# Optimization experiments

Hardware: AMD Instinct MI355X
Metric: run time of the kernel (lower is better)

## Reference

```python
import jax, jax.numpy as jnp
import numpy as np

CONF_THR = 0.2      # confidence_threshold default
NMS_THR = 0.45      # nms_threshold default
TARGET_ID = 0       # NAME2ID['person'] in COCO ordering
CLASS_OFFSET = 1e4  # per-class box offset so cross-class IoU == 0 (per-class NMS)
B, N, C = 4, 8192, 80


def setup_inputs() -> dict:
    key = jax.random.key(0)
    kxy, kwh, kobj, kcls = jax.random.split(key, 4)
    xy = jax.random.uniform(kxy, (B, N, 2)) * 600.0          # x1, y1
    wh = jax.random.uniform(kwh, (B, N, 2)) * 100.0 + 1.0    # box w, h
    boxes = jnp.concatenate([xy, xy + wh], axis=-1)           # x1 y1 x2 y2
    obj = jax.random.uniform(kobj, (B, N, 1))                 # objectness score
    clsp = jax.random.uniform(kcls, (B, N, C))                # class probs
    detection = jnp.concatenate([boxes, obj, clsp], axis=-1)  # [B, N, 5+C]
    return {"detection": detection}


def _pairwise_iou(b):
    # b: [N, 4] in x1y1x2y2
    area = (b[:, 2] - b[:, 0]) * (b[:, 3] - b[:, 1])
    lt = jnp.maximum(b[:, None, :2], b[None, :, :2])
    rb = jnp.minimum(b[:, None, 2:], b[None, :, 2:])
    wh = jnp.clip(rb - lt, 0.0)
    inter = wh[..., 0] * wh[..., 1]
    return inter / (area[:, None] + area[None, :] - inter + 1e-9)


def _nms_image(boxes, scores, classprobs, labels):
    # Fixed-shape, masked equivalent of the torch per-image filter+per-class NMS.
    valid = (scores > CONF_THR) & (labels == TARGET_ID)
    s = jnp.where(valid, scores, -1.0)
    order = jnp.argsort(-s)  # descending score (NMS visiting order)
    b = boxes[order]
    s = s[order]
    cp = classprobs[order]
    lb = labels[order]
    v = valid[order]
    # Offset boxes per class label -> IoU between different classes is 0,
    # which exactly reproduces the per-class NMS loop.
    ob = b + lb.astype(b.dtype)[:, None] * CLASS_OFFSET
    iou = _pairwise_iou(ob)  # [N, N]

    def step(keep, xs):
        row, i, vi = xs
        suppressed = jnp.any(keep & (row > NMS_THR))
        k = vi & jnp.logical_not(suppressed)
        return keep.at[i].set(k), k

    _, keep = jax.lax.scan(
        step, jnp.zeros(s.shape[0], dtype=bool), (iou, jnp.arange(s.shape[0]), v)
    )
    # Compact kept detections to the front (stable sort preserves descending score
    # order among kept boxes, matching the final argsort in torch).
    s_rank = jnp.where(keep, s, -1.0)
    final = jnp.argsort(-s_rank)
    kf = keep[final]
    m = kf.astype(b.dtype)
    out_boxes = b[final] * m[:, None]
    out_scores = jnp.where(kf, s[final], 0.0)
    out_classprobs = cp[final] * m
    out_labels = jnp.where(kf, lb[final], -1)
    return out_boxes, out_scores, out_classprobs, out_labels


def reference(detection):
    # split_detections
    boxes = detection[..., :4]           # [B, N, 4]
    scores = detection[..., 4]           # [B, N]
    cls = detection[..., 5:]             # [B, N, C]
    classprobs = jnp.max(cls, axis=-1)
    labels = jnp.argmax(cls, axis=-1)
    # filter_detections, batched over images
    return jax.vmap(_nms_image)(boxes, scores, classprobs, labels)
```

## Files before the change

### kernel.cpp

```cpp
#include <hip/hip_runtime.h>
#include <cstdint>
#include <cstddef>

typedef unsigned long long u64;

#define BB 4
#define NN 8192
#define DSTRIDE 85
#define RPB 64
#define BPI 128
#define NBLK (BB * BPI)
#define RCAP 64
#define SCAP 256
#define CONF_THRF 0.2f
#define NMS_THRF 0.45f
#define PLANE (BB * NN)

__global__ __launch_bounds__(256) void scan_kernel(
    const float* __restrict__ det, float* __restrict__ out,
    int* __restrict__ counts, float* __restrict__ cand) {
  __shared__ int wcnt[4];
  const int tid = threadIdx.x;
  const int blk = blockIdx.x;
  const int r = tid >> 2, q = tid & 3;
  const int row = blk * RPB + r;
  const float* d = det + (size_t)row * DSTRIDE;

  float best = -1.0f; int barg = 0;
  const float* cb = d + 5 + 20 * q;
#pragma unroll
  for (int k = 0; k < 5; ++k) {
    float4 v = *reinterpret_cast<const float4*>(cb + 4 * k);
    int c0 = 20 * q + 4 * k;
    if (v.x > best) { best = v.x; barg = c0; }
    if (v.y > best) { best = v.y; barg = c0 + 1; }
    if (v.z > best) { best = v.z; barg = c0 + 2; }
    if (v.w > best) { best = v.w; barg = c0 + 3; }
  }
#pragma unroll
  for (int off = 1; off <= 2; off <<= 1) {
    float ov = __shfl_xor(best, off);
    int   oa = __shfl_xor(barg, off);
    if (ov > best || (ov == best && oa < barg)) { best = ov; barg = oa; }
  }

  float4 box = make_float4(0.f, 0.f, 0.f, 0.f);
  float score = 0.f;
  bool valid = false;
  if (q == 0) {
    box = *reinterpret_cast<const float4*>(d);
    score = d[4];
    valid = (score > CONF_THRF) && (barg == 0);
  }

  const int base = blk * RPB;
  if (tid < 64) {
    reinterpret_cast<float4*>(out)[base + tid] = make_float4(0.f, 0.f, 0.f, 0.f);
  } else if (tid < 128) {
    out[(size_t)PLANE * 4 + base + (tid - 64)] = 0.f;
  } else if (tid < 192) {
    out[(size_t)PLANE * 5 + base + (tid - 128)] = 0.f;
  } else {
    out[(size_t)PLANE * 6 + base + (tid - 192)] = -1.0f;
  }

  u64 mask = __ballot(valid);
  const int wave = tid >> 6, lane = tid & 63;
  if (lane == 0) wcnt[wave] = __popcll(mask);
  __syncthreads();
  if (valid) {
    int offw = (wave > 0 ? wcnt[0] : 0) + (wave > 1 ? wcnt[1] : 0) +
               (wave > 2 ? wcnt[2] : 0);
    int pos = __popcll(mask & ((1ull << lane) - 1ull));
    float* p = cand + ((size_t)blk * RCAP + (offw + pos)) * 8;
    reinterpret_cast<float4*>(p)[0] = box;
    reinterpret_cast<float4*>(p)[1] =
        make_float4(score, best, __int_as_float(row & (NN - 1)), 0.f);
  }
  if (tid == 0) counts[blk] = wcnt[0] + wcnt[1] + wcnt[2] + wcnt[3];
}

__global__ __launch_bounds__(256) void nms_kernel(
    float* __restrict__ out, const int* __restrict__ counts,
    const float* __restrict__ cand) {
  __shared__ int cnt[BPI];
  __shared__ float ux1[SCAP], uy1[SCAP], ux2[SCAP], uy2[SCAP];
  __shared__ float usc[SCAP], ucp[SCAP];
  __shared__ u64 keys[SCAP];
  __shared__ float sx1[SCAP], sy1[SCAP], sx2[SCAP], sy2[SCAP];
  __shared__ float sar[SCAP], ssc[SCAP], scp[SCAP];
  __shared__ u64 mat[SCAP][4];

  const int b = blockIdx.x, tid = threadIdx.x;

  int c0 = 0;
  if (tid < BPI) { c0 = counts[b * BPI + tid]; cnt[tid] = c0; }
  __syncthreads();
  for (int s = 1; s < BPI; s <<= 1) {
    int v = 0;
    if (tid < BPI) { v = cnt[tid]; if (tid >= s) v += cnt[tid - s]; }
    __syncthreads();
    if (tid < BPI) cnt[tid] = v;
    __syncthreads();
  }
  int K = cnt[BPI - 1];
  if (K > SCAP) K = SCAP;

  if (tid < BPI && c0 > 0) {
    int off = cnt[tid] - c0;
    const float4* p = reinterpret_cast<const float4*>(
        cand + ((size_t)(b * BPI + tid)) * RCAP * 8);
    for (int k = 0; k < c0; ++k) {
      int o = off + k;
      if (o < SCAP) {
        float4 v0 = p[2 * k], v1 = p[2 * k + 1];
        ux1[o] = v0.x; uy1[o] = v0.y; ux2[o] = v0.z; uy2[o] = v0.w;
        usc[o] = v1.x; ucp[o] = v1.y;
        int idx = __float_as_int(v1.z);
        keys[o] = ((u64)__float_as_uint(v1.x) << 32) |
                  ((u64)(unsigned)(0xFFFF - idx) << 16) | (unsigned)o;
      }
    }
  }
  __syncthreads();

  if (tid < K) {
    u64 my = keys[tid];
    int r = 0;
    for (int s = 0; s < K; ++s) r += (keys[s] > my) ? 1 : 0;
    float x1 = ux1[tid], y1 = uy1[tid], x2 = ux2[tid], y2 = uy2[tid];
    sx1[r] = x1; sy1[r] = y1; sx2[r] = x2; sy2[r] = y2;
    sar[r] = (x2 - x1) * (y2 - y1);
    ssc[r] = usc[tid]; scp[r] = ucp[tid];
  }
  __syncthreads();

  const int W = (K + 63) >> 6;
  for (int t = tid; t < K * 4; t += 256) {
    int i = t >> 2, w = t & 3;
    u64 word = 0;
    if (w < W) {
      float ax1 = sx1[i], ay1 = sy1[i], ax2 = sx2[i], ay2 = sy2[i], aa = sar[i];
      int j0 = w * 64;
      int jend = min(K, j0 + 64);
      for (int j = max(j0, i + 1); j < jend; ++j) {
        float xx1 = fmaxf(ax1, sx1[j]);
        float yy1 = fmaxf(ay1, sy1[j]);
        float xx2 = fminf(ax2, sx2[j]);
        float yy2 = fminf(ay2, sy2[j]);
        float wi = fmaxf(xx2 - xx1, 0.f);
        float hi = fmaxf(yy2 - yy1, 0.f);
        float inter = wi * hi;
        float iou = inter / (aa + sar[j] - inter + 1e-9f);
        if (iou > NMS_THRF) word |= 1ull << (j - j0);
      }
    }
    mat[i][w] = word;
  }
  __syncthreads();

  u64 rem0 = 0, rem1 = 0, rem2 = 0, rem3 = 0;
  u64 kp0 = 0, kp1 = 0, kp2 = 0, kp3 = 0;
#define GREEDY_CHUNK(WW, REMW, KPW)                                        \
  for (int ii = 0; ii < 64; ++ii) {                                        \
    int i = (WW) * 64 + ii;                                                \
    if (i >= K) break;                                                     \
    u64 m0 = mat[i][0], m1 = mat[i][1], m2 = mat[i][2], m3 = mat[i][3];    \
    if (!((REMW >> ii) & 1ull)) {                                          \
      KPW |= 1ull << ii;                                                   \
      rem0 |= m0; rem1 |= m1; rem2 |= m2; rem3 |= m3;                      \
    }                                                                      \
  }
  GREEDY_CHUNK(0, rem0, kp0)
  GREEDY_CHUNK(1, rem1, kp1)
  GREEDY_CHUNK(2, rem2, kp2)
  GREEDY_CHUNK(3, rem3, kp3)
#undef GREEDY_CHUNK

  if (tid < K) {
    int wi = tid >> 6, bi = tid & 63;
    u64 kw = (wi == 0) ? kp0 : (wi == 1) ? kp1 : (wi == 2) ? kp2 : kp3;
    if ((kw >> bi) & 1ull) {
      int r = (wi > 0 ? __popcll(kp0) : 0) + (wi > 1 ? __popcll(kp1) : 0) +
              (wi > 2 ? __popcll(kp2) : 0) +
              __popcll(kw & ((1ull << bi) - 1ull));
      size_t o = (size_t)b * NN + r;
      reinterpret_cast<float4*>(out)[o] =
          make_float4(sx1[tid], sy1[tid], sx2[tid], sy2[tid]);
      out[(size_t)PLANE * 4 + o] = ssc[tid];
      out[(size_t)PLANE * 5 + o] = scp[tid];
      out[(size_t)PLANE * 6 + o] = 0.0f;
    }
  }
}

extern "C" void kernel_launch(void* const* d_in, const int* in_sizes, int n_in,
                              void* d_out, int out_size, void* d_ws, size_t ws_size,
                              hipStream_t stream) {
  const float* det = (const float*)d_in[0];
  float* out = (float*)d_out;
  int* counts = (int*)d_ws;
  float* cand = (float*)((char*)d_ws + 2048);

  scan_kernel<<<NBLK, 256, 0, stream>>>(det, out, counts, cand);
  nms_kernel<<<BB, 256, 0, stream>>>(out, counts, cand);
}
```

Before: 84.41 us.

## Fuse scan and NMS into one kernel with last-block flag wait

Merges the per-row scan and the per-image NMS into a single launch. Each block publishes its candidate count with a marker through an atomic release store, and the last block then polls these flags and runs NMS for all four images, one wave per image, synchronising with wave barriers only. Input rows are staged through LDS before the class argmax, and the candidate cap drops from 256 to 192. The aim is to remove the second launch and the inter-kernel gap. The cost is that all NMS work is serialised onto one block, and the fixed marker is never cleared between calls, so stale flags in the workspace can let the last block read counts before this call's blocks have written them.

```diff
diff --git a/kernel.cpp b/kernel.cpp
--- a/kernel.cpp
+++ b/kernel.cpp
@@ -11,48 +11,62 @@
 #define BPI 128
 #define NBLK (BB * BPI)
 #define RCAP 64
-#define SCAP 256
+#define SCAP 192
 #define CONF_THRF 0.2f
 #define NMS_THRF 0.45f
 #define PLANE (BB * NN)
-
-__global__ __launch_bounds__(256) void scan_kernel(
+#define IMSZ 16640
+#define MARK 0x5EED
+
+__device__ __forceinline__ void wave_fence() {
+  __asm__ volatile("" ::: "memory");
+  __builtin_amdgcn_wave_barrier();
+  __asm__ volatile("" ::: "memory");
+}
+
+__global__ __launch_bounds__(256) void fused_kernel(
     const float* __restrict__ det, float* __restrict__ out,
     int* __restrict__ counts, float* __restrict__ cand) {
+  __shared__ __align__(16) char arena[4 * IMSZ];
   __shared__ int wcnt[4];
   const int tid = threadIdx.x;
   const int blk = blockIdx.x;
+  const int wave = tid >> 6, lane = tid & 63;
+
+  {
+    const float4* src =
+        reinterpret_cast<const float4*>(det + (size_t)blk * (RPB * DSTRIDE));
+    float4* dst = reinterpret_cast<float4*>(arena);
+    for (int i = tid; i < (RPB * DSTRIDE) / 4; i += 256) dst[i] = src[i];
+  }
+  __syncthreads();
+
+  const float* st = reinterpret_cast<const float*>(arena);
   const int r = tid >> 2, q = tid & 3;
-  const int row = blk * RPB + r;
-  const float* d = det + (size_t)row * DSTRIDE;
-
   float best = -1.0f; int barg = 0;
-  const float* cb = d + 5 + 20 * q;
-#pragma unroll
-  for (int k = 0; k < 5; ++k) {
-    float4 v = *reinterpret_cast<const float4*>(cb + 4 * k);
-    int c0 = 20 * q + 4 * k;
-    if (v.x > best) { best = v.x; barg = c0; }
-    if (v.y > best) { best = v.y; barg = c0 + 1; }
-    if (v.z > best) { best = v.z; barg = c0 + 2; }
-    if (v.w > best) { best = v.w; barg = c0 + 3; }
+  {
+    const float* rowp = st + r * DSTRIDE + 5 + 20 * q;
+#pragma unroll
+    for (int k = 0; k < 20; ++k) {
+      float v = rowp[k];
+      if (v > best) { best = v; barg = 20 * q + k; }
+    }
   }
 #pragma unroll
   for (int off = 1; off <= 2; off <<= 1) {
     float ov = __shfl_xor(best, off);
-    int   oa = __shfl_xor(barg, off);
+    int oa = __shfl_xor(barg, off);
     if (ov > best || (ov == best && oa < barg)) { best = ov; barg = oa; }
   }
-
   float4 box = make_float4(0.f, 0.f, 0.f, 0.f);
   float score = 0.f;
   bool valid = false;
   if (q == 0) {
-    box = *reinterpret_cast<const float4*>(d);
-    score = d[4];
+    const float* rp = st + r * DSTRIDE;
+    box = make_float4(rp[0], rp[1], rp[2], rp[3]);
+    score = rp[4];
     valid = (score > CONF_THRF) && (barg == 0);
   }
-
   const int base = blk * RPB;
   if (tid < 64) {
     reinterpret_cast<float4*>(out)[base + tid] = make_float4(0.f, 0.f, 0.f, 0.f);
@@ -63,132 +77,157 @@
   } else {
     out[(size_t)PLANE * 6 + base + (tid - 192)] = -1.0f;
   }
-
   u64 mask = __ballot(valid);
-  const int wave = tid >> 6, lane = tid & 63;
   if (lane == 0) wcnt[wave] = __popcll(mask);
   __syncthreads();
+  int bcount = wcnt[0] + wcnt[1] + wcnt[2] + wcnt[3];
   if (valid) {
     int offw = (wave > 0 ? wcnt[0] : 0) + (wave > 1 ? wcnt[1] : 0) +
                (wave > 2 ? wcnt[2] : 0);
     int pos = __popcll(mask & ((1ull << lane) - 1ull));
-    float* p = cand + ((size_t)blk * RCAP + (offw + pos)) * 8;
-    reinterpret_cast<float4*>(p)[0] = box;
-    reinterpret_cast<float4*>(p)[1] =
-        make_float4(score, best, __int_as_float(row & (NN - 1)), 0.f);
-  }
-  if (tid == 0) counts[blk] = wcnt[0] + wcnt[1] + wcnt[2] + wcnt[3];
-}
-
-__global__ __launch_bounds__(256) void nms_kernel(
-    float* __restrict__ out, const int* __restrict__ counts,
-    const float* __restrict__ cand) {
-  __shared__ int cnt[BPI];
-  __shared__ float ux1[SCAP], uy1[SCAP], ux2[SCAP], uy2[SCAP];
-  __shared__ float usc[SCAP], ucp[SCAP];
-  __shared__ u64 keys[SCAP];
-  __shared__ float sx1[SCAP], sy1[SCAP], sx2[SCAP], sy2[SCAP];
-  __shared__ float sar[SCAP], ssc[SCAP], scp[SCAP];
-  __shared__ u64 mat[SCAP][4];
-
-  const int b = blockIdx.x, tid = threadIdx.x;
-
-  int c0 = 0;
-  if (tid < BPI) { c0 = counts[b * BPI + tid]; cnt[tid] = c0; }
+    float4* p =
+        reinterpret_cast<float4*>(cand + ((size_t)blk * RCAP + offw + pos) * 8);
+    p[0] = box;
+    p[1] = make_float4(score, best,
+                       __int_as_float((blk & (BPI - 1)) * RPB + r), 0.f);
+  }
   __syncthreads();
-  for (int s = 1; s < BPI; s <<= 1) {
-    int v = 0;
-    if (tid < BPI) { v = cnt[tid]; if (tid >= s) v += cnt[tid - s]; }
-    __syncthreads();
-    if (tid < BPI) cnt[tid] = v;
-    __syncthreads();
-  }
-  int K = cnt[BPI - 1];
+  if (tid == 0)
+    __hip_atomic_store(&counts[blk], (MARK << 16) | bcount, __ATOMIC_RELEASE,
+                       __HIP_MEMORY_SCOPE_AGENT);
+
+  if (blk != NBLK - 1) return;
+
+  const int img = wave;
+  char* A = arena + img * IMSZ;
+  u64* keys = reinterpret_cast<u64*>(A);
+  u64* mat = reinterpret_cast<u64*>(A + 1536);
+  float* ux1 = reinterpret_cast<float*>(A + 6144);
+  float* uy1 = reinterpret_cast<float*>(A + 6912);
+  float* ux2 = reinterpret_cast<float*>(A + 7680);
+  float* uy2 = reinterpret_cast<float*>(A + 8448);
+  float* usc = reinterpret_cast<float*>(A + 9216);
+  float* ucp = reinterpret_cast<float*>(A + 9984);
+  float* sx1 = reinterpret_cast<float*>(A + 10752);
+  float* sy1 = reinterpret_cast<float*>(A + 11520);
+  float* sx2 = reinterpret_cast<float*>(A + 12288);
+  float* sy2 = reinterpret_cast<float*>(A + 13056);
+  float* sar = reinterpret_cast<float*>(A + 13824);
+  float* ssc = reinterpret_cast<float*>(A + 14592);
+  float* scp = reinterpret_cast<float*>(A + 15360);
+
+  const int m0 = img * BPI + lane, m1 = m0 + 64;
+  int v0, v1;
+  do {
+    v0 = __hip_atomic_load(&counts[m0], __ATOMIC_ACQUIRE,
+                           __HIP_MEMORY_SCOPE_AGENT);
+  } while ((v0 >> 16) != MARK);
+  do {
+    v1 = __hip_atomic_load(&counts[m1], __ATOMIC_ACQUIRE,
+                           __HIP_MEMORY_SCOPE_AGENT);
+  } while ((v1 >> 16) != MARK);
+  int c0 = v0 & 0xFFFF, c1 = v1 & 0xFFFF;
+
+  int s0 = c0;
+#pragma unroll
+  for (int d = 1; d < 64; d <<= 1) {
+    int t = __shfl_up(s0, d);
+    if (lane >= d) s0 += t;
+  }
+  int tot0 = __shfl(s0, 63);
+  int s1 = c1;
+#pragma unroll
+  for (int d = 1; d < 64; d <<= 1) {
+    int t = __shfl_up(s1, d);
+    if (lane >= d) s1 += t;
+  }
+  s1 += tot0;
+  int K = __shfl(s1, 63);
   if (K > SCAP) K = SCAP;
-
-  if (tid < BPI && c0 > 0) {
-    int off = cnt[tid] - c0;
-    const float4* p = reinterpret_cast<const float4*>(
-        cand + ((size_t)(b * BPI + tid)) * RCAP * 8);
-    for (int k = 0; k < c0; ++k) {
-      int o = off + k;
+  int e0 = s0 - c0, e1 = s1 - c1;
+
+#pragma unroll
+  for (int pass = 0; pass < 2; ++pass) {
+    int m = pass ? m1 : m0;
+    int c = pass ? c1 : c0;
+    int e = pass ? e1 : e0;
+    const float4* p = reinterpret_cast<const float4*>(cand + (size_t)m * RCAP * 8);
+    for (int k = 0; k < c; ++k) {
+      int o = e + k;
       if (o < SCAP) {
-        float4 v0 = p[2 * k], v1 = p[2 * k + 1];
-        ux1[o] = v0.x; uy1[o] = v0.y; ux2[o] = v0.z; uy2[o] = v0.w;
-        usc[o] = v1.x; ucp[o] = v1.y;
-        int idx = __float_as_int(v1.z);
-        keys[o] = ((u64)__float_as_uint(v1.x) << 32) |
+        float4 a = p[2 * k], bq = p[2 * k + 1];
+        ux1[o] = a.x; uy1[o] = a.y; ux2[o] = a.z; uy2[o] = a.w;
+        usc[o] = bq.x; ucp[o] = bq.y;
+        int idx = __float_as_int(bq.z);
+        keys[o] = ((u64)__float_as_uint(bq.x) << 32) |
                   ((u64)(unsigned)(0xFFFF - idx) << 16) | (unsigned)o;
       }
     }
   }
-  __syncthreads();
-
-  if (tid < K) {
-    u64 my = keys[tid];
-    int r = 0;
-    for (int s = 0; s < K; ++s) r += (keys[s] > my) ? 1 : 0;
-    float x1 = ux1[tid], y1 = uy1[tid], x2 = ux2[tid], y2 = uy2[tid];
-    sx1[r] = x1; sy1[r] = y1; sx2[r] = x2; sy2[r] = y2;
-    sar[r] = (x2 - x1) * (y2 - y1);
-    ssc[r] = usc[tid]; scp[r] = ucp[tid];
-  }
-  __syncthreads();
-
-  const int W = (K + 63) >> 6;
-  for (int t = tid; t < K * 4; t += 256) {
-    int i = t >> 2, w = t & 3;
-    u64 word = 0;
-    if (w < W) {
-      float ax1 = sx1[i], ay1 = sy1[i], ax2 = sx2[i], ay2 = sy2[i], aa = sar[i];
-      int j0 = w * 64;
-      int jend = min(K, j0 + 64);
-      for (int j = max(j0, i + 1); j < jend; ++j) {
-        float xx1 = fmaxf(ax1, sx1[j]);
-        float yy1 = fmaxf(ay1, sy1[j]);
-        float xx2 = fminf(ax2, sx2[j]);
-        float yy2 = fminf(ay2, sy2[j]);
-        float wi = fmaxf(xx2 - xx1, 0.f);
-        float hi = fmaxf(yy2 - yy1, 0.f);
-        float inter = wi * hi;
-        float iou = inter / (aa + sar[j] - inter + 1e-9f);
-        if (iou > NMS_THRF) word |= 1ull << (j - j0);
+  wave_fence();
+
+  for (int o = lane; o < K; o += 64) {
+    u64 my = keys[o];
+    int rr = 0;
+    for (int s = 0; s < K; ++s) rr += (keys[s] > my) ? 1 : 0;
+    float x1 = ux1[o], y1 = uy1[o], x2 = ux2[o], y2 = uy2[o];
+    sx1[rr] = x1; sy1[rr] = y1; sx2[rr] = x2; sy2[rr] = y2;
+    sar[rr] = (x2 - x1) * (y2 - y1);
+    ssc[rr] = usc[o]; scp[rr] = ucp[o];
+  }
+  wave_fence();
+
+  for (int i = lane; i < K; i += 64) {
+    float ax1 = sx1[i], ay1 = sy1[i], ax2 = sx2[i], ay2 = sy2[i], aa = sar[i];
+    u64 w0 = 0, w1 = 0, w2 = 0;
+    for (int j = i + 1; j < K; ++j) {
+      float xx1 = fmaxf(ax1, sx1[j]);
+      float yy1 = fmaxf(ay1, sy1[j]);
+      float xx2 = fminf(ax2, sx2[j]);
+      float yy2 = fminf(ay2, sy2[j]);
+      float w = fmaxf(xx2 - xx1, 0.f);
+      float h = fmaxf(yy2 - yy1, 0.f);
+      float inter = w * h;
+      float iou = inter / (aa + sar[j] - inter + 1e-9f);
+      if (iou > NMS_THRF) {
+        u64 bit = 1ull << (j & 63);
+        int wj = j >> 6;
+        w0 |= (wj == 0) ? bit : 0;
+        w1 |= (wj == 1) ? bit : 0;
+        w2 |= (wj == 2) ? bit : 0;
       }
     }
-    mat[i][w] = word;
-  }
-  __syncthreads();
-
-  u64 rem0 = 0, rem1 = 0, rem2 = 0, rem3 = 0;
-  u64 kp0 = 0, kp1 = 0, kp2 = 0, kp3 = 0;
-#define GREEDY_CHUNK(WW, REMW, KPW)                                        \
-  for (int ii = 0; ii < 64; ++ii) {                                        \
-    int i = (WW) * 64 + ii;                                                \
-    if (i >= K) break;                                                     \
-    u64 m0 = mat[i][0], m1 = mat[i][1], m2 = mat[i][2], m3 = mat[i][3];    \
-    if (!((REMW >> ii) & 1ull)) {                                          \
-      KPW |= 1ull << ii;                                                   \
-      rem0 |= m0; rem1 |= m1; rem2 |= m2; rem3 |= m3;                      \
-    }                                                                      \
+    mat[i * 3] = w0; mat[i * 3 + 1] = w1; mat[i * 3 + 2] = w2;
+  }
+  wave_fence();
+
+  u64 rem0 = 0, rem1 = 0, rem2 = 0, kp0 = 0, kp1 = 0, kp2 = 0;
+#define GREEDY_CHUNK(WW, REMW, KPW)                                      \
+  for (int ii = 0; ii < 64; ++ii) {                                      \
+    int i = (WW) * 64 + ii;                                              \
+    if (i >= K) break;                                                   \
+    u64 g0 = mat[i * 3], g1 = mat[i * 3 + 1], g2 = mat[i * 3 + 2];       \
+    if (!((REMW >> ii) & 1ull)) {                                        \
+      KPW |= 1ull << ii;                                                 \
+      rem0 |= g0; rem1 |= g1; rem2 |= g2;                                \
+    }                                                                    \
   }
   GREEDY_CHUNK(0, rem0, kp0)
   GREEDY_CHUNK(1, rem1, kp1)
   GREEDY_CHUNK(2, rem2, kp2)
-  GREEDY_CHUNK(3, rem3, kp3)
 #undef GREEDY_CHUNK
 
-  if (tid < K) {
-    int wi = tid >> 6, bi = tid & 63;
-    u64 kw = (wi == 0) ? kp0 : (wi == 1) ? kp1 : (wi == 2) ? kp2 : kp3;
+  for (int i = lane; i < K; i += 64) {
+    int wi = i >> 6, bi = i & 63;
+    u64 kw = (wi == 0) ? kp0 : (wi == 1) ? kp1 : kp2;
     if ((kw >> bi) & 1ull) {
-      int r = (wi > 0 ? __popcll(kp0) : 0) + (wi > 1 ? __popcll(kp1) : 0) +
-              (wi > 2 ? __popcll(kp2) : 0) +
-              __popcll(kw & ((1ull << bi) - 1ull));
-      size_t o = (size_t)b * NN + r;
+      int rr = (wi > 0 ? __popcll(kp0) : 0) + (wi > 1 ? __popcll(kp1) : 0) +
+               __popcll(kw & ((1ull << bi) - 1ull));
+      size_t o = (size_t)img * NN + rr;
       reinterpret_cast<float4*>(out)[o] =
-          make_float4(sx1[tid], sy1[tid], sx2[tid], sy2[tid]);
-      out[(size_t)PLANE * 4 + o] = ssc[tid];
-      out[(size_t)PLANE * 5 + o] = scp[tid];
+          make_float4(sx1[i], sy1[i], sx2[i], sy2[i]);
+      out[(size_t)PLANE * 4 + o] = ssc[i];
+      out[(size_t)PLANE * 5 + o] = scp[i];
       out[(size_t)PLANE * 6 + o] = 0.0f;
     }
   }
@@ -202,6 +241,5 @@
   int* counts = (int*)d_ws;
   float* cand = (float*)((char*)d_ws + 2048);
 
-  scan_kernel<<<NBLK, 256, 0, stream>>>(det, out, counts, cand);
-  nms_kernel<<<BB, 256, 0, stream>>>(out, counts, cand);
+  fused_kernel<<<NBLK, 256, 0, stream>>>(det, out, counts, cand);
 }
```

Measured after the change: 97.01 us. 14.9% more time.
